# Kernel optimization log

Hardware: AMD Instinct MI355X
Metric: run time of the kernel (lower is better)

Reference implementation:

```python
import jax, jax.numpy as jnp
import numpy as np

B, L, D = 4, 2048, 512
H = 8
DK = D // H
FACTOR = 5
SK = FACTOR * int(np.ceil(np.log(L)))  # sample_k = u = 40
NTOP = FACTOR * int(np.ceil(np.log(L)))  # U_part = 40


def setup_inputs() -> dict:
    key = jax.random.key(0)
    ks = jax.random.split(key, 12)
    s = 1.0 / np.sqrt(D)
    return {
        "queries": jax.random.normal(ks[0], (B, L, D), jnp.float32),
        "keys": jax.random.normal(ks[1], (B, L, D), jnp.float32),
        "values": jax.random.normal(ks[2], (B, L, D), jnp.float32),
        "attn_mask": jnp.zeros((1,), jnp.bool_),
        "index_sample": jax.random.randint(ks[3], (L, SK), 0, L),
        "Wq": jax.random.normal(ks[4], (D, D), jnp.float32) * s,
        "bq": jnp.zeros((D,), jnp.float32),
        "Wk": jax.random.normal(ks[5], (D, D), jnp.float32) * s,
        "bk": jnp.zeros((D,), jnp.float32),
        "Wv": jax.random.normal(ks[6], (D, D), jnp.float32) * s,
        "bv": jnp.zeros((D,), jnp.float32),
        "Wo": jax.random.normal(ks[7], (D, D), jnp.float32) * s,
        "bo": jnp.zeros((D,), jnp.float32),
    }


def reference(queries, keys, values, attn_mask, index_sample, Wq, bq, Wk, bk, Wv, bv, Wo, bo):
    b, l, d = queries.shape
    s = keys.shape[1]
    # projections: [B,L,D] -> [B,H,L,dk]
    Q = (queries @ Wq + bq).reshape(b, l, H, DK).transpose(0, 2, 1, 3)
    K = (keys @ Wk + bk).reshape(b, s, H, DK).transpose(0, 2, 1, 3)
    V = (values @ Wv + bv).reshape(b, s, H, DK).transpose(0, 2, 1, 3)
    # --- _prob_QK: sampled QK scores ---
    K_samp = K[:, :, index_sample, :]                       # [B,H,L,SK,DK]
    QKs = jnp.einsum('bhqe,bhqje->bhqj', Q, K_samp)        # [B,H,L,SK]
    M = QKs.max(-1) - QKs.sum(-1) / s                       # sparsity measure
    _, M_top = jax.lax.top_k(M, NTOP)                       # [B,H,NTOP]
    Q_red = jnp.take_along_axis(Q, M_top[..., None], axis=2)  # [B,H,NTOP,DK]
    scores = jnp.einsum('bhue,bhse->bhus', Q_red, K)        # [B,H,NTOP,S]
    scale = 1.0 / np.sqrt(DK)
    scores = scores * scale
    # --- initial context (mask_flag=False): V summed over keys ---
    ctx = jnp.broadcast_to(V.sum(axis=2, keepdims=True), (b, H, l, DK))
    # --- update context at selected queries ---
    attn = jax.nn.softmax(scores, axis=-1)
    upd = jnp.einsum('bhus,bhsd->bhud', attn, V)            # [B,H,NTOP,DK]
    b_idx = jnp.arange(b)[:, None, None]
    h_idx = jnp.arange(H)[None, :, None]
    ctx = ctx.at[b_idx, h_idx, M_top].set(upd)
    out = ctx.transpose(0, 2, 1, 3).reshape(b, l, d) @ Wo + bo
    return out
```

## Files before the change

### kernel.cpp

```cpp
#include <hip/hip_runtime.h>


typedef unsigned short u16;
typedef unsigned long long u64;
typedef __attribute__((ext_vector_type(8))) short short8;
typedef __attribute__((ext_vector_type(4))) float f32x4;

constexpr int NB = 4;
constexpr int SEQ = 2048;
constexpr int DM = 512;
constexpr int NH = 8;
constexpr int DH = 64;
constexpr int NS = 40;
constexpr int NT = 40;
constexpr int ROWS = NB * SEQ;
constexpr int BHROWS = NB * NH * SEQ;
constexpr int NSC = 8;
constexpr int VCH = 16;

__device__ __forceinline__ u16 f2bf(float x) {
  union { float f; unsigned u; } v; v.f = x;
  unsigned r = v.u + 0x7FFFu + ((v.u >> 16) & 1u);
  return (u16)(r >> 16);
}
__device__ __forceinline__ float bf2f(u16 b) {
  union { unsigned u; float f; } v; v.u = ((unsigned)b) << 16;
  return v.f;
}

__device__ __forceinline__ void gload16(void* lds, const void* g) {
  __builtin_amdgcn_global_load_lds(
      (const __attribute__((address_space(1))) unsigned int*)g,
      (__attribute__((address_space(3))) unsigned int*)lds, 16, 0, 0);
}

__global__ __launch_bounds__(256) void cvt_split_all(const float* __restrict__ q,
                                                     const float* __restrict__ k,
                                                     const float* __restrict__ v,
                                                     u16* __restrict__ QXH, u16* __restrict__ QXL,
                                                     u16* __restrict__ KXH, u16* __restrict__ KXL,
                                                     u16* __restrict__ VXH) {
  const int i = blockIdx.x * 256 + threadIdx.x;
  const int z = blockIdx.z;
  const float* X = (z == 0) ? q : (z == 1) ? k : v;
  u16* H = (z == 0) ? QXH : (z == 1) ? KXH : VXH;
  u16* L = (z == 0) ? QXL : KXL;
  float4 val = ((const float4*)X)[i];
  ushort4 h;
  h.x = f2bf(val.x); h.y = f2bf(val.y); h.z = f2bf(val.z); h.w = f2bf(val.w);
  ((ushort4*)H)[i] = h;
  if (z < 2) {
    ushort4 l;
    l.x = f2bf(val.x - bf2f(h.x)); l.y = f2bf(val.y - bf2f(h.y));
    l.z = f2bf(val.z - bf2f(h.z)); l.w = f2bf(val.w - bf2f(h.w));
    ((ushort4*)L)[i] = l;
  }
}

__global__ __launch_bounds__(256) void cvt_wt_all(const float* __restrict__ Wq,
                                                  const float* __restrict__ Wk,
                                                  const float* __restrict__ Wv,
                                                  const float* __restrict__ Wo,
                                                  u16* __restrict__ WqH, u16* __restrict__ WqL,
                                                  u16* __restrict__ WkH, u16* __restrict__ WkL,
                                                  u16* __restrict__ WvH, u16* __restrict__ WoH) {
  __shared__ float T[64][65];
  const int z = blockIdx.z;
  const float* W = (z == 0) ? Wq : (z == 1) ? Wk : (z == 2) ? Wv : Wo;
  u16* H = (z == 0) ? WqH : (z == 1) ? WkH : (z == 2) ? WvH : WoH;
  u16* L = (z == 0) ? WqL : WkL;
  const int doLo = (z < 2);
  const int c0 = blockIdx.x * 64;
  const int r0 = blockIdx.y * 64;
  const int t = threadIdx.x;
  const int lr = t >> 4, lc4 = (t & 15) * 4;
#pragma unroll
  for (int i = 0; i < 4; i++) {
    float4 val = *(const float4*)&W[(size_t)(r0 + lr + i * 16) * DM + c0 + lc4];
    T[lr + i * 16][lc4 + 0] = val.x;
    T[lr + i * 16][lc4 + 1] = val.y;
    T[lr + i * 16][lc4 + 2] = val.z;
    T[lr + i * 16][lc4 + 3] = val.w;
  }
  __syncthreads();
#pragma unroll
  for (int i = 0; i < 4; i++) {
    const int n = lr + i * 16;
    float x0 = T[lc4 + 0][n], x1 = T[lc4 + 1][n], x2 = T[lc4 + 2][n], x3 = T[lc4 + 3][n];
    ushort4 h;
    h.x = f2bf(x0); h.y = f2bf(x1); h.z = f2bf(x2); h.w = f2bf(x3);
    *(ushort4*)&H[(size_t)(c0 + n) * DM + r0 + lc4] = h;
    if (doLo) {
      ushort4 l;
      l.x = f2bf(x0 - bf2f(h.x)); l.y = f2bf(x1 - bf2f(h.y));
      l.z = f2bf(x2 - bf2f(h.z)); l.w = f2bf(x3 - bf2f(h.w));
      *(ushort4*)&L[(size_t)(c0 + n) * DM + r0 + lc4] = l;
    }
  }
}

template <bool SPLIT3, bool TOSPLIT>
__device__ __forceinline__ void gemm_body128(const u16* __restrict__ XH,
                                             const u16* __restrict__ XL,
                                             const u16* __restrict__ WTH,
                                             const u16* __restrict__ WTL,
                                             const float* __restrict__ bias,
                                             float* __restrict__ out,
                                             u16* Ah, u16* Al, u16* Bh, u16* Bl,
                                             int row0, int col0) {
  const int tid = threadIdx.x, lane = tid & 63, w = tid >> 6;
  const int wr = (w >> 1) * 64, wc = (w & 1) * 64;
  const int lr = lane & 15, kb8 = (lane >> 4) * 8;
  const int mrow = lane >> 2;
  const int kcol = (lane & 3) * 8;

  f32x4 acc[4][4];
#pragma unroll
  for (int i = 0; i < 4; i++)
#pragma unroll
    for (int j = 0; j < 4; j++) acc[i][j] = (f32x4){0.f, 0.f, 0.f, 0.f};

  constexpr int PER = SPLIT3 ? 8 : 4;

  for (int k0 = 0; k0 < DM; k0 += 32) {
    __syncthreads();
#pragma unroll
    for (int i = 0; i < PER; i++) {
      const int c = w * PER + i;
      const u16* g;
      u16* l;
      if (SPLIT3) {
        if (c < 8)       { g = XH  + (size_t)(row0 + c * 16 + mrow) * DM + k0 + kcol;        l = Ah + c * 512; }
        else if (c < 16) { g = XL  + (size_t)(row0 + (c - 8) * 16 + mrow) * DM + k0 + kcol;  l = Al + (c - 8) * 512; }
        else if (c < 24) { g = WTH + (size_t)(col0 + (c - 16) * 16 + mrow) * DM + k0 + kcol; l = Bh + (c - 16) * 512; }
        else             { g = WTL + (size_t)(col0 + (c - 24) * 16 + mrow) * DM + k0 + kcol; l = Bl + (c - 24) * 512; }
      } else {
        if (c < 8)       { g = XH  + (size_t)(row0 + c * 16 + mrow) * DM + k0 + kcol;        l = Ah + c * 512; }
        else             { g = WTH + (size_t)(col0 + (c - 8) * 16 + mrow) * DM + k0 + kcol;  l = Bh + (c - 8) * 512; }
      }
      gload16(l, g);
    }
    __syncthreads();

    short8 ah[4], bh[4];
#pragma unroll
    for (int i = 0; i < 4; i++) ah[i] = *(const short8*)&Ah[(wr + i * 16 + lr) * 32 + kb8];
#pragma unroll
    for (int j = 0; j < 4; j++) bh[j] = *(const short8*)&Bh[(wc + j * 16 + lr) * 32 + kb8];
    if constexpr (SPLIT3) {
      short8 al[4], bl[4];
#pragma unroll
      for (int i = 0; i < 4; i++) al[i] = *(const short8*)&Al[(wr + i * 16 + lr) * 32 + kb8];
#pragma unroll
      for (int j = 0; j < 4; j++) bl[j] = *(const short8*)&Bl[(wc + j * 16 + lr) * 32 + kb8];
#pragma unroll
      for (int i = 0; i < 4; i++)
#pragma unroll
        for (int j = 0; j < 4; j++) {
          acc[i][j] = __builtin_amdgcn_mfma_f32_16x16x32_bf16(ah[i], bh[j], acc[i][j], 0, 0, 0);
          acc[i][j] = __builtin_amdgcn_mfma_f32_16x16x32_bf16(ah[i], bl[j], acc[i][j], 0, 0, 0);
          acc[i][j] = __builtin_amdgcn_mfma_f32_16x16x32_bf16(al[i], bh[j], acc[i][j], 0, 0, 0);
        }
    } else {
#pragma unroll
      for (int i = 0; i < 4; i++)
#pragma unroll
        for (int j = 0; j < 4; j++)
          acc[i][j] = __builtin_amdgcn_mfma_f32_16x16x32_bf16(ah[i], bh[j], acc[i][j], 0, 0, 0);
    }
  }

#pragma unroll
  for (int i = 0; i < 4; i++)
#pragma unroll
    for (int j = 0; j < 4; j++) {
      const int col = col0 + wc + j * 16 + lr;
      const float bval = bias[col];
#pragma unroll
      for (int r = 0; r < 4; r++) {
        const int row = row0 + wr + i * 16 + (lane >> 4) * 4 + r;
        const float v = acc[i][j][r] + bval;
        if constexpr (TOSPLIT) {
          const int b = row >> 11, l2 = row & (SEQ - 1);
          const int h = col >> 6, dk = col & 63;
          out[((size_t)(b * NH + h) * SEQ + l2) * DH + dk] = v;
        } else {
          out[(size_t)row * DM + col] = v;
        }
      }
    }
}

template <bool SPLIT3, bool TOSPLIT>
__device__ __forceinline__ void gemm_body64(const u16* __restrict__ XH,
                                            const u16* __restrict__ XL,
                                            const u16* __restrict__ WTH,
                                            const u16* __restrict__ WTL,
                                            const float* __restrict__ bias,
                                            float* __restrict__ out,
                                            u16* Ah, u16* Al, u16* Bh, u16* Bl,
                                            int row0, int col0) {
  const int tid = threadIdx.x, lane = tid & 63, w = tid >> 6;
  const int wr = (w >> 1) * 64, wc = (w & 1) * 32;
  const int lr = lane & 15, kb8 = (lane >> 4) * 8;
  const int mrow = lane >> 2;
  const int kcol = (lane & 3) * 8;

  f32x4 acc[4][2];
#pragma unroll
  for (int i = 0; i < 4; i++)
#pragma unroll
    for (int j = 0; j < 2; j++) acc[i][j] = (f32x4){0.f, 0.f, 0.f, 0.f};

  constexpr int PER = SPLIT3 ? 6 : 3;

  for (int k0 = 0; k0 < DM; k0 += 32) {
    __syncthreads();
#pragma unroll
    for (int i = 0; i < PER; i++) {
      const int c = w * PER + i;
      const u16* g;
      u16* l;
      if (SPLIT3) {
        if (c < 8)       { g = XH  + (size_t)(row0 + c * 16 + mrow) * DM + k0 + kcol;        l = Ah + c * 512; }
        else if (c < 16) { g = XL  + (size_t)(row0 + (c - 8) * 16 + mrow) * DM + k0 + kcol;  l = Al + (c - 8) * 512; }
        else if (c < 20) { g = WTH + (size_t)(col0 + (c - 16) * 16 + mrow) * DM + k0 + kcol; l = Bh + (c - 16) * 512; }
        else             { g = WTL + (size_t)(col0 + (c - 20) * 16 + mrow) * DM + k0 + kcol; l = Bl + (c - 20) * 512; }
      } else {
        if (c < 8)       { g = XH  + (size_t)(row0 + c * 16 + mrow) * DM + k0 + kcol;        l = Ah + c * 512; }
        else             { g = WTH + (size_t)(col0 + (c - 8) * 16 + mrow) * DM + k0 + kcol;  l = Bh + (c - 8) * 512; }
      }
      gload16(l, g);
    }
    __syncthreads();

    short8 ah[4], bh[2];
#pragma unroll
    for (int i = 0; i < 4; i++) ah[i] = *(const short8*)&Ah[(wr + i * 16 + lr) * 32 + kb8];
#pragma unroll
    for (int j = 0; j < 2; j++) bh[j] = *(const short8*)&Bh[(wc + j * 16 + lr) * 32 + kb8];
    if constexpr (SPLIT3) {
      short8 al[4], bl[2];
#pragma unroll
      for (int i = 0; i < 4; i++) al[i] = *(const short8*)&Al[(wr + i * 16 + lr) * 32 + kb8];
#pragma unroll
      for (int j = 0; j < 2; j++) bl[j] = *(const short8*)&Bl[(wc + j * 16 + lr) * 32 + kb8];
#pragma unroll
      for (int i = 0; i < 4; i++)
#pragma unroll
        for (int j = 0; j < 2; j++) {
          acc[i][j] = __builtin_amdgcn_mfma_f32_16x16x32_bf16(ah[i], bh[j], acc[i][j], 0, 0, 0);
          acc[i][j] = __builtin_amdgcn_mfma_f32_16x16x32_bf16(ah[i], bl[j], acc[i][j], 0, 0, 0);
          acc[i][j] = __builtin_amdgcn_mfma_f32_16x16x32_bf16(al[i], bh[j], acc[i][j], 0, 0, 0);
        }
    } else {
#pragma unroll
      for (int i = 0; i < 4; i++)
#pragma unroll
        for (int j = 0; j < 2; j++)
          acc[i][j] = __builtin_amdgcn_mfma_f32_16x16x32_bf16(ah[i], bh[j], acc[i][j], 0, 0, 0);
    }
  }

#pragma unroll
  for (int i = 0; i < 4; i++)
#pragma unroll
    for (int j = 0; j < 2; j++) {
      const int col = col0 + wc + j * 16 + lr;
      const float bval = bias[col];
#pragma unroll
      for (int r = 0; r < 4; r++) {
        const int row = row0 + wr + i * 16 + (lane >> 4) * 4 + r;
        const float v = acc[i][j][r] + bval;
        if constexpr (TOSPLIT) {
          const int b = row >> 11, l2 = row & (SEQ - 1);
          const int h = col >> 6, dk = col & 63;
          out[((size_t)(b * NH + h) * SEQ + l2) * DH + dk] = v;
        } else {
          out[(size_t)row * DM + col] = v;
        }
      }
    }
}

__global__ __launch_bounds__(256) void gemm_proj(const u16* __restrict__ QXH, const u16* __restrict__ QXL,
                                                 const u16* __restrict__ KXH, const u16* __restrict__ KXL,
                                                 const u16* __restrict__ VXH,
                                                 const u16* __restrict__ WqH, const u16* __restrict__ WqL,
                                                 const u16* __restrict__ WkH, const u16* __restrict__ WkL,
                                                 const u16* __restrict__ WvH,
                                                 const float* __restrict__ bq, const float* __restrict__ bk,
                                                 const float* __restrict__ bv,
                                                 float* __restrict__ Q, float* __restrict__ Kp,
                                                 float* __restrict__ Vp) {
  __shared__ __align__(16) u16 Ah[128 * 32];
  __shared__ __align__(16) u16 Al[128 * 32];
  __shared__ __align__(16) u16 Bh[128 * 32];
  __shared__ __align__(16) u16 Bl[128 * 32];
  const int row0 = blockIdx.x * 128, col0 = blockIdx.y * 128;
  if (blockIdx.z == 0)
    gemm_body128<true, true>(QXH, QXL, WqH, WqL, bq, Q, Ah, Al, Bh, Bl, row0, col0);
  else if (blockIdx.z == 1)
    gemm_body128<true, true>(KXH, KXL, WkH, WkL, bk, Kp, Ah, Al, Bh, Bl, row0, col0);
  else
    gemm_body128<false, true>(VXH, VXH, WvH, WvH, bv, Vp, Ah, Al, Bh, Bl, row0, col0);
}

__global__ __launch_bounds__(256) void gemm_out(const u16* __restrict__ CH,
                                                const u16* __restrict__ WoH,
                                                const float* __restrict__ bo,
                                                float* __restrict__ out) {
  __shared__ __align__(16) u16 Ah[128 * 32];
  __shared__ __align__(16) u16 Al[128 * 32];
  __shared__ __align__(16) u16 Bh[64 * 32];
  __shared__ __align__(16) u16 Bl[64 * 32];
  gemm_body64<false, false>(CH, CH, WoH, WoH, bo, out, Ah, Al, Bh, Bl,
                            blockIdx.x * 128, blockIdx.y * 64);
}

__global__ __launch_bounds__(256) void m_kernel(const float* __restrict__ Q,
                                                const float* __restrict__ K,
                                                const int* __restrict__ idxs,
                                                float* __restrict__ M) {
  __shared__ int idl[4 * NS];
  const int tid = threadIdx.x;
  const int x = blockIdx.x & 7;
  const int slot = blockIdx.x >> 3;
  const int bh = x * 4 + (slot >> 9);
  const int q0 = (slot & 511) * 4;

  if (tid < 4 * NS) idl[tid] = idxs[q0 * NS + tid];
  __syncthreads();

  const int lane = tid & 63, wid = tid >> 6;
  const int r = bh * SEQ + q0 + wid;
  const int g = lane >> 3;
  const int d8 = (lane & 7) * 8;
  const float* Qr = Q + (size_t)r * DH + d8;
  const float4 q0v = *(const float4*)Qr;
  const float4 q1v = *(const float4*)(Qr + 4);
  const float* Kbh = K + (size_t)bh * SEQ * DH;

  int ks[5];
#pragma unroll
  for (int p = 0; p < 5; p++) ks[p] = idl[wid * NS + g + 8 * p];
  float4 k0[5], k1[5];
#pragma unroll
  for (int p = 0; p < 5; p++) {
    const float* Kr = Kbh + (size_t)ks[p] * DH + d8;
    k0[p] = *(const float4*)Kr;
    k1[p] = *(const float4*)(Kr + 4);
  }
  float mx = -1e30f, sm = 0.f;
#pragma unroll
  for (int p = 0; p < 5; p++) {
    float acc = q0v.x * k0[p].x + q0v.y * k0[p].y + q0v.z * k0[p].z + q0v.w * k0[p].w +
                q1v.x * k1[p].x + q1v.y * k1[p].y + q1v.z * k1[p].z + q1v.w * k1[p].w;
    acc += __shfl_xor(acc, 1, 64);
    acc += __shfl_xor(acc, 2, 64);
    acc += __shfl_xor(acc, 4, 64);
    mx = fmaxf(mx, acc);
    sm += acc;
  }
#pragma unroll
  for (int o = 8; o <= 32; o <<= 1) {
    mx = fmaxf(mx, __shfl_xor(mx, o, 64));
    sm += __shfl_xor(sm, o, 64);
  }
  if (lane == 0) M[r] = mx - sm * (1.0f / (float)SEQ);
}

__global__ __launch_bounds__(1024) void topk_kernel(const float* __restrict__ M,
                                                    int* __restrict__ Mtop) {
  __shared__ u64 keys[SEQ];
  const int bh = blockIdx.x, tid = threadIdx.x;
  const float* Mb = M + (size_t)bh * SEQ;
#pragma unroll
  for (int i = tid; i < SEQ; i += 1024) {
    unsigned ub = __float_as_uint(Mb[i]);
    ub ^= (ub >> 31) ? 0xFFFFFFFFu : 0x80000000u;
    keys[i] = ((u64)ub << 32) | (u64)(unsigned)~i;
  }
  __syncthreads();
  for (int k = 2; k <= SEQ; k <<= 1) {
    for (int j = k >> 1; j > 0; j >>= 1) {
#pragma unroll
      for (int i = tid; i < SEQ; i += 1024) {
        const int partner = i ^ j;
        if (partner > i) {
          const u64 a = keys[i], b = keys[partner];
          const bool desc = ((i & k) == 0);
          if (desc ? (a < b) : (a > b)) { keys[i] = b; keys[partner] = a; }
        }
      }
      __syncthreads();
    }
  }
  if (tid < NT) Mtop[bh * NT + tid] = (int)~(unsigned)keys[tid];
}

__global__ __launch_bounds__(256) void vsum1_kernel(const float* __restrict__ V,
                                                    float* __restrict__ part) {
  __shared__ float sm[4][DH];
  const int bh = blockIdx.x, c = blockIdx.y, tid = threadIdx.x;
  const int dk = tid & 63, p = tid >> 6;
  const float* Vb = V + ((size_t)bh * SEQ + c * (SEQ / VCH)) * DH;
  float s = 0.f;
  for (int l = p; l < SEQ / VCH; l += 4) s += Vb[(size_t)l * DH + dk];
  sm[p][dk] = s;
  __syncthreads();
  if (p == 0)
    part[(size_t)(bh * VCH + c) * DH + dk] = sm[0][dk] + sm[1][dk] + sm[2][dk] + sm[3][dk];
}

__global__ __launch_bounds__(64) void vsum2_kernel(const float* __restrict__ part,
                                                   float* __restrict__ Vsum) {
  const int bh = blockIdx.x, dk = threadIdx.x;
  float s = 0.f;
#pragma unroll
  for (int c = 0; c < VCH; c++) s += part[(size_t)(bh * VCH + c) * DH + dk];
  Vsum[bh * DH + dk] = s;
}

__global__ __launch_bounds__(256) void ctxinit_kernel(const float* __restrict__ Vsum,
                                                      u16* __restrict__ CH) {
  const int idx = blockIdx.x * 256 + threadIdx.x;
  const int f = idx * 4;
  const int d = f & (DM - 1), b = f >> 20;
  float4 v = *(const float4*)&Vsum[b * DM + d];
  ushort4 h;
  h.x = f2bf(v.x); h.y = f2bf(v.y); h.z = f2bf(v.z); h.w = f2bf(v.w);
  ((ushort4*)CH)[idx] = h;
}

__global__ __launch_bounds__(256) void scores_kernel(const float* __restrict__ Q,
                                                     const float* __restrict__ K,
                                                     const int* __restrict__ Mtop,
                                                     float* __restrict__ scores) {
  __shared__ float Qs[NT * DH];
  const int bh = blockIdx.x, tid = threadIdx.x;
  for (int i = tid; i < NT * DH; i += 256) {
    int u = i >> 6, dk = i & 63;
    int row = Mtop[bh * NT + u];
    Qs[i] = Q[((size_t)bh * SEQ + row) * DH + dk];
  }
  __syncthreads();
  const int s = blockIdx.y * 256 + tid;
  const float* Krow = K + ((size_t)bh * SEQ + s) * DH;
  float4 kr[16];
#pragma unroll
  for (int g = 0; g < 16; g++) kr[g] = *(const float4*)&Krow[g * 4];
  for (int u = 0; u < NT; u++) {
    float acc = 0.f;
#pragma unroll
    for (int g = 0; g < 16; g++) {
      float4 qv = *(const float4*)&Qs[u * DH + g * 4];
      acc = fmaf(qv.x, kr[g].x, acc);
      acc = fmaf(qv.y, kr[g].y, acc);
      acc = fmaf(qv.z, kr[g].z, acc);
      acc = fmaf(qv.w, kr[g].w, acc);
    }
    scores[((size_t)bh * NT + u) * SEQ + s] = acc * 0.125f;
  }
}

__global__ __launch_bounds__(256) void stats_kernel(const float* __restrict__ scores,
                                                    float* __restrict__ mstat) {
  __shared__ float red[256];
  const int row = blockIdx.x, tid = threadIdx.x;
  const float* p = scores + (size_t)row * SEQ;
  float4 v0 = *(const float4*)&p[tid * 4];
  float4 v1 = *(const float4*)&p[1024 + tid * 4];
  float mx = fmaxf(fmaxf(fmaxf(v0.x, v0.y), fmaxf(v0.z, v0.w)),
                   fmaxf(fmaxf(v1.x, v1.y), fmaxf(v1.z, v1.w)));
  red[tid] = mx;
  __syncthreads();
  for (int s = 128; s; s >>= 1) {
    if (tid < s) red[tid] = fmaxf(red[tid], red[tid + s]);
    __syncthreads();
  }
  mx = red[0];
  __syncthreads();
  float sm = __expf(v0.x - mx) + __expf(v0.y - mx) + __expf(v0.z - mx) + __expf(v0.w - mx) +
             __expf(v1.x - mx) + __expf(v1.y - mx) + __expf(v1.z - mx) + __expf(v1.w - mx);
  red[tid] = sm;
  __syncthreads();
  for (int s = 128; s; s >>= 1) {
    if (tid < s) red[tid] += red[tid + s];
    __syncthreads();
  }
  if (tid == 0) {
    mstat[row * 2] = mx;
    mstat[row * 2 + 1] = 1.0f / red[0];
  }
}

__global__ __launch_bounds__(256) void pv_partial_kernel(const float* __restrict__ scores,
                                                         const float* __restrict__ V,
                                                         const float* __restrict__ mstat,
                                                         float* __restrict__ updp) {
  __shared__ float Vl[64 * DH];
  __shared__ float Al2[NT * 64];
  __shared__ float smx[NT], sden[NT];
  const int bh = blockIdx.x, sc = blockIdx.y, tid = threadIdx.x;
  const int s0 = sc * 256;
  const int wid = tid >> 6, dk = tid & 63;
  float acc[10] = {};

  if (tid < NT) {
    smx[tid] = mstat[(bh * NT + tid) * 2];
    sden[tid] = mstat[(bh * NT + tid) * 2 + 1];
  }
  __syncthreads();

  for (int st = 0; st < 4; st++) {
    const int sb = s0 + st * 64;
    __syncthreads();
#pragma unroll
    for (int i = 0; i < 16; i++) {
      int idx = tid + i * 256;
      int sj = idx >> 6, d2 = idx & 63;
      Vl[idx] = V[((size_t)bh * SEQ + sb + sj) * DH + d2];
    }
#pragma unroll
    for (int i = 0; i < 10; i++) {
      int idx = tid + i * 256;
      int u = idx >> 6, sj = idx & 63;
      float s = scores[((size_t)bh * NT + u) * SEQ + sb + sj];
      Al2[idx] = __expf(s - smx[u]) * sden[u];
    }
    __syncthreads();
    for (int g = 0; g < 16; g++) {
      float a[10][4];
#pragma unroll
      for (int i = 0; i < 10; i++) {
        float4 t = *(const float4*)&Al2[(wid + 4 * i) * 64 + g * 4];
        a[i][0] = t.x; a[i][1] = t.y; a[i][2] = t.z; a[i][3] = t.w;
      }
#pragma unroll
      for (int t = 0; t < 4; t++) {
        float v = Vl[(g * 4 + t) * DH + dk];
#pragma unroll
        for (int i = 0; i < 10; i++) acc[i] = fmaf(a[i][t], v, acc[i]);
      }
    }
  }

#pragma unroll
  for (int i = 0; i < 10; i++) {
    int u = wid + 4 * i;
    updp[((size_t)(bh * NSC + sc) * NT + u) * DH + dk] = acc[i];
  }
}

__global__ __launch_bounds__(256) void reduce_scatter_kernel(const float* __restrict__ updp,
                                                             const int* __restrict__ Mtop,
                                                             u16* __restrict__ CH) {
  const int bh = blockIdx.x;
  const int u = blockIdx.y * 4 + (threadIdx.x >> 6);
  const int dk = threadIdx.x & 63;
  float s = 0.f;
#pragma unroll
  for (int sc = 0; sc < NSC; sc++)
    s += updp[((size_t)(bh * NSC + sc) * NT + u) * DH + dk];
  const int row = Mtop[bh * NT + u];
  const int b = bh >> 3, h = bh & 7;
  CH[((size_t)b * SEQ + row) * DM + h * DH + dk] = f2bf(s);
}

extern "C" void kernel_launch(void* const* d_in, const int* in_sizes, int n_in,
                              void* d_out, int out_size, void* d_ws, size_t ws_size,
                              hipStream_t stream) {
  (void)in_sizes; (void)n_in; (void)out_size; (void)ws_size;
  const float* queries = (const float*)d_in[0];
  const float* keys    = (const float*)d_in[1];
  const float* values  = (const float*)d_in[2];
  const int* index_sample = (const int*)d_in[4];
  const float* Wq = (const float*)d_in[5];
  const float* bq = (const float*)d_in[6];
  const float* Wk = (const float*)d_in[7];
  const float* bk = (const float*)d_in[8];
  const float* Wv = (const float*)d_in[9];
  const float* bv = (const float*)d_in[10];
  const float* Wo = (const float*)d_in[11];
  const float* bo = (const float*)d_in[12];
  float* out = (float*)d_out;

  float* ws = (float*)d_ws;
  float* Q      = ws;
  float* Kp     = Q + (size_t)ROWS * DM;
  float* Vp     = Kp + (size_t)ROWS * DM;
  float* scores = Vp + (size_t)ROWS * DM;
  float* M      = scores + (size_t)NB * NH * NT * SEQ;
  float* Vsum   = M + BHROWS;
  float* vpart  = Vsum + NB * NH * DH;
  float* mstat  = vpart + NB * NH * VCH * DH;
  float* updp   = mstat + NB * NH * NT * 2;
  int*   Mtop   = (int*)(updp + (size_t)NSC * NB * NH * NT * DH);
  u16* QXH = (u16*)(Mtop + NB * NH * NT + 64);
  u16* QXL = QXH + (size_t)ROWS * DM;
  u16* KXH = QXL + (size_t)ROWS * DM;
  u16* KXL = KXH + (size_t)ROWS * DM;
  u16* VXH = KXL + (size_t)ROWS * DM;
  u16* CH  = VXH + (size_t)ROWS * DM;
  u16* WqH = CH + (size_t)ROWS * DM;
  u16* WqL = WqH + (size_t)DM * DM;
  u16* WkH = WqL + (size_t)DM * DM;
  u16* WkL = WkH + (size_t)DM * DM;
  u16* WvH = WkL + (size_t)DM * DM;
  u16* WoH = WvH + (size_t)DM * DM;

  const int n4x = ROWS * DM / 4;

  cvt_wt_all<<<dim3(8, 8, 4), 256, 0, stream>>>(Wq, Wk, Wv, Wo,
                                                WqH, WqL, WkH, WkL, WvH, WoH);
  cvt_split_all<<<dim3(n4x / 256, 1, 3), 256, 0, stream>>>(queries, keys, values,
                                                           QXH, QXL, KXH, KXL, VXH);
  gemm_proj<<<dim3(ROWS / 128, DM / 128, 3), 256, 0, stream>>>(
      QXH, QXL, KXH, KXL, VXH, WqH, WqL, WkH, WkL, WvH, bq, bk, bv, Q, Kp, Vp);

  m_kernel<<<BHROWS / 4, 256, 0, stream>>>(Q, Kp, index_sample, M);
  topk_kernel<<<NB * NH, 1024, 0, stream>>>(M, Mtop);
  vsum1_kernel<<<dim3(NB * NH, VCH), 256, 0, stream>>>(Vp, vpart);
  vsum2_kernel<<<NB * NH, 64, 0, stream>>>(vpart, Vsum);
  ctxinit_kernel<<<(ROWS * DM / 4) / 256, 256, 0, stream>>>(Vsum, CH);
  scores_kernel<<<dim3(NB * NH, SEQ / 256), 256, 0, stream>>>(Q, Kp, Mtop, scores);
  stats_kernel<<<NB * NH * NT, 256, 0, stream>>>(scores, mstat);
  pv_partial_kernel<<<dim3(NB * NH, NSC), 256, 0, stream>>>(scores, Vp, mstat, updp);
  reduce_scatter_kernel<<<dim3(NB * NH, NT / 4), 256, 0, stream>>>(updp, Mtop, CH);

  gemm_out<<<dim3(ROWS / 128, DM / 64), 256, 0, stream>>>(CH, WoH, bo, out);
}
```

Before: 204.5 us.

## Fuse scores, softmax stats and PV into one kernel; merge conversion kernels

Replaces the separate scores, stats and PV-partial kernels with one kernel that computes QK scores for a 256-key chunk, exponentiates them into LDS, accumulates per-chunk denominators and PV partials, then normalizes in the reduce-scatter step. This removes the global scores buffer round trip and two launches. It drops max-subtraction in the softmax, which risks overflow for large scores. The weight and activation conversion kernels are also merged into one launch.

```diff
diff --git a/kernel.cpp b/kernel.cpp
--- a/kernel.cpp
+++ b/kernel.cpp
@@ -34,45 +34,46 @@
       (__attribute__((address_space(3))) unsigned int*)lds, 16, 0, 0);
 }
 
-__global__ __launch_bounds__(256) void cvt_split_all(const float* __restrict__ q,
-                                                     const float* __restrict__ k,
-                                                     const float* __restrict__ v,
-                                                     u16* __restrict__ QXH, u16* __restrict__ QXL,
-                                                     u16* __restrict__ KXH, u16* __restrict__ KXL,
-                                                     u16* __restrict__ VXH) {
-  const int i = blockIdx.x * 256 + threadIdx.x;
-  const int z = blockIdx.z;
-  const float* X = (z == 0) ? q : (z == 1) ? k : v;
-  u16* H = (z == 0) ? QXH : (z == 1) ? KXH : VXH;
-  u16* L = (z == 0) ? QXL : KXL;
-  float4 val = ((const float4*)X)[i];
-  ushort4 h;
-  h.x = f2bf(val.x); h.y = f2bf(val.y); h.z = f2bf(val.z); h.w = f2bf(val.w);
-  ((ushort4*)H)[i] = h;
-  if (z < 2) {
-    ushort4 l;
-    l.x = f2bf(val.x - bf2f(h.x)); l.y = f2bf(val.y - bf2f(h.y));
-    l.z = f2bf(val.z - bf2f(h.z)); l.w = f2bf(val.w - bf2f(h.w));
-    ((ushort4*)L)[i] = l;
-  }
-}
-
-__global__ __launch_bounds__(256) void cvt_wt_all(const float* __restrict__ Wq,
-                                                  const float* __restrict__ Wk,
-                                                  const float* __restrict__ Wv,
-                                                  const float* __restrict__ Wo,
-                                                  u16* __restrict__ WqH, u16* __restrict__ WqL,
-                                                  u16* __restrict__ WkH, u16* __restrict__ WkL,
-                                                  u16* __restrict__ WvH, u16* __restrict__ WoH) {
+__global__ __launch_bounds__(256) void cvt_all(const float* __restrict__ q,
+                                               const float* __restrict__ k,
+                                               const float* __restrict__ v,
+                                               const float* __restrict__ Wq,
+                                               const float* __restrict__ Wk,
+                                               const float* __restrict__ Wv,
+                                               const float* __restrict__ Wo,
+                                               u16* __restrict__ QXH, u16* __restrict__ QXL,
+                                               u16* __restrict__ KXH, u16* __restrict__ KXL,
+                                               u16* __restrict__ VXH,
+                                               u16* __restrict__ WqH, u16* __restrict__ WqL,
+                                               u16* __restrict__ WkH, u16* __restrict__ WkL,
+                                               u16* __restrict__ WvH, u16* __restrict__ WoH) {
   __shared__ float T[64][65];
-  const int z = blockIdx.z;
-  const float* W = (z == 0) ? Wq : (z == 1) ? Wk : (z == 2) ? Wv : Wo;
-  u16* H = (z == 0) ? WqH : (z == 1) ? WkH : (z == 2) ? WvH : WoH;
-  u16* L = (z == 0) ? WqL : WkL;
-  const int doLo = (z < 2);
-  const int c0 = blockIdx.x * 64;
-  const int r0 = blockIdx.y * 64;
-  const int t = threadIdx.x;
+  const int z = blockIdx.z, t = threadIdx.x;
+  if (z < 3) {
+    const int i = blockIdx.x * 256 + t;
+    const float* X = (z == 0) ? q : (z == 1) ? k : v;
+    u16* H = (z == 0) ? QXH : (z == 1) ? KXH : VXH;
+    u16* L = (z == 0) ? QXL : KXL;
+    float4 val = ((const float4*)X)[i];
+    ushort4 h;
+    h.x = f2bf(val.x); h.y = f2bf(val.y); h.z = f2bf(val.z); h.w = f2bf(val.w);
+    ((ushort4*)H)[i] = h;
+    if (z < 2) {
+      ushort4 l;
+      l.x = f2bf(val.x - bf2f(h.x)); l.y = f2bf(val.y - bf2f(h.y));
+      l.z = f2bf(val.z - bf2f(h.z)); l.w = f2bf(val.w - bf2f(h.w));
+      ((ushort4*)L)[i] = l;
+    }
+    return;
+  }
+  if (blockIdx.x >= 256) return;
+  const int wz = blockIdx.x >> 6;
+  const int c0 = (blockIdx.x & 7) * 64;
+  const int r0 = ((blockIdx.x >> 3) & 7) * 64;
+  const float* W = (wz == 0) ? Wq : (wz == 1) ? Wk : (wz == 2) ? Wv : Wo;
+  u16* H = (wz == 0) ? WqH : (wz == 1) ? WkH : (wz == 2) ? WvH : WoH;
+  u16* L = (wz == 0) ? WqL : WkL;
+  const int doLo = (wz < 2);
   const int lr = t >> 4, lc4 = (t & 15) * 4;
 #pragma unroll
   for (int i = 0; i < 4; i++) {
@@ -433,113 +434,73 @@
   ((ushort4*)CH)[idx] = h;
 }
 
-__global__ __launch_bounds__(256) void scores_kernel(const float* __restrict__ Q,
-                                                     const float* __restrict__ K,
-                                                     const int* __restrict__ Mtop,
-                                                     float* __restrict__ scores) {
-  __shared__ float Qs[NT * DH];
-  const int bh = blockIdx.x, tid = threadIdx.x;
+__global__ __launch_bounds__(256) void pv_fused_kernel(const float* __restrict__ Q,
+                                                       const float* __restrict__ K,
+                                                       const float* __restrict__ V,
+                                                       const int* __restrict__ Mtop,
+                                                       float* __restrict__ updp,
+                                                       float* __restrict__ dpart) {
+  __shared__ float El[NT * 256];
+  __shared__ float QV[4096];
+  const int bh = blockIdx.x, sc = blockIdx.y, tid = threadIdx.x;
+  const int s0 = sc * 256;
+  const int wid = tid >> 6, lane = tid & 63;
+
   for (int i = tid; i < NT * DH; i += 256) {
     int u = i >> 6, dk = i & 63;
     int row = Mtop[bh * NT + u];
-    Qs[i] = Q[((size_t)bh * SEQ + row) * DH + dk];
-  }
+    QV[i] = Q[((size_t)bh * SEQ + row) * DH + dk];
+  }
+  const float* Krow = K + ((size_t)bh * SEQ + s0 + tid) * DH;
+  float4 kr[16];
+#pragma unroll
+  for (int g = 0; g < 16; g++) kr[g] = *(const float4*)&Krow[g * 4];
   __syncthreads();
-  const int s = blockIdx.y * 256 + tid;
-  const float* Krow = K + ((size_t)bh * SEQ + s) * DH;
-  float4 kr[16];
-#pragma unroll
-  for (int g = 0; g < 16; g++) kr[g] = *(const float4*)&Krow[g * 4];
+
   for (int u = 0; u < NT; u++) {
     float acc = 0.f;
 #pragma unroll
     for (int g = 0; g < 16; g++) {
-      float4 qv = *(const float4*)&Qs[u * DH + g * 4];
+      float4 qv = *(const float4*)&QV[u * DH + g * 4];
       acc = fmaf(qv.x, kr[g].x, acc);
       acc = fmaf(qv.y, kr[g].y, acc);
       acc = fmaf(qv.z, kr[g].z, acc);
       acc = fmaf(qv.w, kr[g].w, acc);
     }
-    scores[((size_t)bh * NT + u) * SEQ + s] = acc * 0.125f;
-  }
-}
-
-__global__ __launch_bounds__(256) void stats_kernel(const float* __restrict__ scores,
-                                                    float* __restrict__ mstat) {
-  __shared__ float red[256];
-  const int row = blockIdx.x, tid = threadIdx.x;
-  const float* p = scores + (size_t)row * SEQ;
-  float4 v0 = *(const float4*)&p[tid * 4];
-  float4 v1 = *(const float4*)&p[1024 + tid * 4];
-  float mx = fmaxf(fmaxf(fmaxf(v0.x, v0.y), fmaxf(v0.z, v0.w)),
-                   fmaxf(fmaxf(v1.x, v1.y), fmaxf(v1.z, v1.w)));
-  red[tid] = mx;
+    El[u * 256 + tid] = __expf(acc * 0.125f);
+  }
   __syncthreads();
-  for (int s = 128; s; s >>= 1) {
-    if (tid < s) red[tid] = fmaxf(red[tid], red[tid + s]);
-    __syncthreads();
-  }
-  mx = red[0];
-  __syncthreads();
-  float sm = __expf(v0.x - mx) + __expf(v0.y - mx) + __expf(v0.z - mx) + __expf(v0.w - mx) +
-             __expf(v1.x - mx) + __expf(v1.y - mx) + __expf(v1.z - mx) + __expf(v1.w - mx);
-  red[tid] = sm;
-  __syncthreads();
-  for (int s = 128; s; s >>= 1) {
-    if (tid < s) red[tid] += red[tid + s];
-    __syncthreads();
-  }
-  if (tid == 0) {
-    mstat[row * 2] = mx;
-    mstat[row * 2 + 1] = 1.0f / red[0];
-  }
-}
-
-__global__ __launch_bounds__(256) void pv_partial_kernel(const float* __restrict__ scores,
-                                                         const float* __restrict__ V,
-                                                         const float* __restrict__ mstat,
-                                                         float* __restrict__ updp) {
-  __shared__ float Vl[64 * DH];
-  __shared__ float Al2[NT * 64];
-  __shared__ float smx[NT], sden[NT];
-  const int bh = blockIdx.x, sc = blockIdx.y, tid = threadIdx.x;
-  const int s0 = sc * 256;
-  const int wid = tid >> 6, dk = tid & 63;
+
+#pragma unroll
+  for (int i = 0; i < 10; i++) {
+    const int u = wid + 4 * i;
+    float p = El[u * 256 + lane] + El[u * 256 + 64 + lane] +
+              El[u * 256 + 128 + lane] + El[u * 256 + 192 + lane];
+#pragma unroll
+    for (int o = 1; o <= 32; o <<= 1) p += __shfl_xor(p, o, 64);
+    if (lane == 0) dpart[(bh * NSC + sc) * NT + u] = p;
+  }
+
   float acc[10] = {};
-
-  if (tid < NT) {
-    smx[tid] = mstat[(bh * NT + tid) * 2];
-    sden[tid] = mstat[(bh * NT + tid) * 2 + 1];
-  }
-  __syncthreads();
-
   for (int st = 0; st < 4; st++) {
-    const int sb = s0 + st * 64;
     __syncthreads();
 #pragma unroll
     for (int i = 0; i < 16; i++) {
       int idx = tid + i * 256;
       int sj = idx >> 6, d2 = idx & 63;
-      Vl[idx] = V[((size_t)bh * SEQ + sb + sj) * DH + d2];
-    }
-#pragma unroll
-    for (int i = 0; i < 10; i++) {
-      int idx = tid + i * 256;
-      int u = idx >> 6, sj = idx & 63;
-      float s = scores[((size_t)bh * NT + u) * SEQ + sb + sj];
-      Al2[idx] = __expf(s - smx[u]) * sden[u];
+      QV[idx] = V[((size_t)bh * SEQ + s0 + st * 64 + sj) * DH + d2];
     }
     __syncthreads();
     for (int g = 0; g < 16; g++) {
       float a[10][4];
 #pragma unroll
       for (int i = 0; i < 10; i++) {
-        float4 t = *(const float4*)&Al2[(wid + 4 * i) * 64 + g * 4];
+        float4 t = *(const float4*)&El[(wid + 4 * i) * 256 + st * 64 + g * 4];
         a[i][0] = t.x; a[i][1] = t.y; a[i][2] = t.z; a[i][3] = t.w;
       }
 #pragma unroll
       for (int t = 0; t < 4; t++) {
-        float v = Vl[(g * 4 + t) * DH + dk];
+        float v = QV[(g * 4 + t) * DH + lane];
 #pragma unroll
         for (int i = 0; i < 10; i++) acc[i] = fmaf(a[i][t], v, acc[i]);
       }
@@ -549,23 +510,26 @@
 #pragma unroll
   for (int i = 0; i < 10; i++) {
     int u = wid + 4 * i;
-    updp[((size_t)(bh * NSC + sc) * NT + u) * DH + dk] = acc[i];
+    updp[((size_t)(bh * NSC + sc) * NT + u) * DH + lane] = acc[i];
   }
 }
 
 __global__ __launch_bounds__(256) void reduce_scatter_kernel(const float* __restrict__ updp,
+                                                             const float* __restrict__ dpart,
                                                              const int* __restrict__ Mtop,
                                                              u16* __restrict__ CH) {
   const int bh = blockIdx.x;
   const int u = blockIdx.y * 4 + (threadIdx.x >> 6);
   const int dk = threadIdx.x & 63;
-  float s = 0.f;
-#pragma unroll
-  for (int sc = 0; sc < NSC; sc++)
+  float s = 0.f, d = 0.f;
+#pragma unroll
+  for (int sc = 0; sc < NSC; sc++) {
     s += updp[((size_t)(bh * NSC + sc) * NT + u) * DH + dk];
+    d += dpart[(bh * NSC + sc) * NT + u];
+  }
   const int row = Mtop[bh * NT + u];
   const int b = bh >> 3, h = bh & 7;
-  CH[((size_t)b * SEQ + row) * DM + h * DH + dk] = f2bf(s);
+  CH[((size_t)b * SEQ + row) * DM + h * DH + dk] = f2bf(s / d);
 }
 
 extern "C" void kernel_launch(void* const* d_in, const int* in_sizes, int n_in,
@@ -590,12 +554,11 @@
   float* Q      = ws;
   float* Kp     = Q + (size_t)ROWS * DM;
   float* Vp     = Kp + (size_t)ROWS * DM;
-  float* scores = Vp + (size_t)ROWS * DM;
-  float* M      = scores + (size_t)NB * NH * NT * SEQ;
+  float* M      = Vp + (size_t)ROWS * DM;
   float* Vsum   = M + BHROWS;
   float* vpart  = Vsum + NB * NH * DH;
-  float* mstat  = vpart + NB * NH * VCH * DH;
-  float* updp   = mstat + NB * NH * NT * 2;
+  float* dpart  = vpart + NB * NH * VCH * DH;
+  float* updp   = dpart + (size_t)NSC * NB * NH * NT;
   int*   Mtop   = (int*)(updp + (size_t)NSC * NB * NH * NT * DH);
   u16* QXH = (u16*)(Mtop + NB * NH * NT + 64);
   u16* QXL = QXH + (size_t)ROWS * DM;
@@ -612,10 +575,9 @@
 
   const int n4x = ROWS * DM / 4;
 
-  cvt_wt_all<<<dim3(8, 8, 4), 256, 0, stream>>>(Wq, Wk, Wv, Wo,
-                                                WqH, WqL, WkH, WkL, WvH, WoH);
-  cvt_split_all<<<dim3(n4x / 256, 1, 3), 256, 0, stream>>>(queries, keys, values,
-                                                           QXH, QXL, KXH, KXL, VXH);
+  cvt_all<<<dim3(n4x / 256, 1, 4), 256, 0, stream>>>(
+      queries, keys, values, Wq, Wk, Wv, Wo,
+      QXH, QXL, KXH, KXL, VXH, WqH, WqL, WkH, WkL, WvH, WoH);
   gemm_proj<<<dim3(ROWS / 128, DM / 128, 3), 256, 0, stream>>>(
       QXH, QXL, KXH, KXL, VXH, WqH, WqL, WkH, WkL, WvH, bq, bk, bv, Q, Kp, Vp);
 
@@ -624,10 +586,8 @@
   vsum1_kernel<<<dim3(NB * NH, VCH), 256, 0, stream>>>(Vp, vpart);
   vsum2_kernel<<<NB * NH, 64, 0, stream>>>(vpart, Vsum);
   ctxinit_kernel<<<(ROWS * DM / 4) / 256, 256, 0, stream>>>(Vsum, CH);
-  scores_kernel<<<dim3(NB * NH, SEQ / 256), 256, 0, stream>>>(Q, Kp, Mtop, scores);
-  stats_kernel<<<NB * NH * NT, 256, 0, stream>>>(scores, mstat);
-  pv_partial_kernel<<<dim3(NB * NH, NSC), 256, 0, stream>>>(scores, Vp, mstat, updp);
-  reduce_scatter_kernel<<<dim3(NB * NH, NT / 4), 256, 0, stream>>>(updp, Mtop, CH);
+  pv_fused_kernel<<<dim3(NB * NH, NSC), 256, 0, stream>>>(Q, Kp, Vp, Mtop, updp, dpart);
+  reduce_scatter_kernel<<<dim3(NB * NH, NT / 4), 256, 0, stream>>>(updp, dpart, Mtop, CH);
 
   gemm_out<<<dim3(ROWS / 128, DM / 64), 256, 0, stream>>>(CH, WoH, bo, out);
 }
```

Result: faster. 196.8 us (-3.8%).
